# Kernel tuning notes

Measured on AMD Instinct MI355X. Metric: run time of the kernel, lower is better.

The kernel has to match this reference:

```python
import jax, jax.numpy as jnp
import numpy as np

B, SEQ_LEN, IN_DIM = 16, 1024, 768
R = 0.1
PI = 3.1415926


def conv1d(x, w, b):
    # x: [B,C,L], w: [O,I,3], 'same' padding, stride 1
    y = jax.lax.conv_general_dilated(x, w, window_strides=(1,), padding=[(1, 1)],
                                     dimension_numbers=('NCH', 'OIH', 'NCH'))
    return y + b[None, :, None]


def layernorm_cl(x, g, b, eps=1e-5):
    # torch nn.LayerNorm((C, L)): normalize jointly over the last two dims of [B,C,L]
    m = x.mean(axis=(1, 2), keepdims=True)
    v = x.var(axis=(1, 2), keepdims=True)
    return (x - m) / jnp.sqrt(v + eps) * g[None] + b[None]


def setup_inputs() -> dict:
    key = jax.random.key(0)
    ks = jax.random.split(key, 8)
    D, D2, L = IN_DIM, IN_DIM * 2, SEQ_LEN
    sc1 = 1.0 / np.sqrt(D * 3)
    sc2 = 1.0 / np.sqrt(D2 * 3)
    return {
        'feats': jax.random.normal(ks[0], (B, L, D), dtype=jnp.float32),
        'conv1_w': jax.random.normal(ks[1], (D2, D, 3), dtype=jnp.float32) * sc1,
        'conv1_b': jnp.zeros((D2,), jnp.float32),
        'ln1_w': jnp.ones((D2, L), jnp.float32),
        'ln1_b': jnp.zeros((D2, L), jnp.float32),
        'conv2_w': jax.random.normal(ks[2], (D2, D2, 3), dtype=jnp.float32) * sc2,
        'conv2_b': jnp.zeros((D2,), jnp.float32),
        'ln2_w': jnp.ones((D2, L), jnp.float32),
        'ln2_b': jnp.zeros((D2, L), jnp.float32),
        'conv3_w': jax.random.normal(ks[3], (2, D2, 3), dtype=jnp.float32) * sc2,
        'conv3_b': jnp.zeros((2,), jnp.float32),
        'ln3_w': jnp.ones((2, L), jnp.float32),
        'ln3_b': jnp.zeros((2, L), jnp.float32),
    }


def reference(feats, conv1_w, conv1_b, ln1_w, ln1_b, conv2_w, conv2_b, ln2_w, ln2_b,
              conv3_w, conv3_b, ln3_w, ln3_b):
    # NOTE: original uses nn.LeakyReLU(True) -> negative_slope=1.0, i.e. identity.
    x = jnp.transpose(feats, (0, 2, 1))                 # [B,D,L]
    h = layernorm_cl(conv1d(x, conv1_w, conv1_b), ln1_w, ln1_b)
    h = layernorm_cl(conv1d(h, conv2_w, conv2_b), ln2_w, ln2_b)
    h = layernorm_cl(conv1d(h, conv3_w, conv3_b), ln3_w, ln3_b)  # [B,2,L]
    s = jax.nn.softmax(h[:, 0, :], axis=1)              # [B,L]
    w = jax.nn.softmax(h[:, 1, :], axis=1)              # [B,L]
    # Vectorized over all centers i: std[b,i] = R*L*s[b,i]
    std = R * SEQ_LEN * s                               # [B,L]
    pos = jnp.arange(SEQ_LEN, dtype=feats.dtype)
    diff2 = (pos[None, :] - pos[:, None]) ** 2          # [i_center, j]
    c = (2.0 * PI) ** -0.5
    gauss = c / std[:, :, None] * jnp.exp(-diff2[None] / (1e-05 + 2.0 * std[:, :, None] ** 2))
    gauss = gauss / jnp.max(gauss, axis=2, keepdims=True)
    att = gauss * w[:, None, :]                         # [B,L_center,L]
    out = jnp.einsum('bij,bjd->bid', att, feats)        # [B,L,D]
    return out
```

## Files before the change

### kernel.cpp

```cpp
#include <hip/hip_runtime.h>
#include <hip/hip_bf16.h>
#include <cstdint>

#define B_   16
#define L_   1024
#define D_   768
#define D2_  1536

typedef __attribute__((ext_vector_type(8))) short bf16x8;
typedef __attribute__((ext_vector_type(4))) float f32x4;

__device__ __forceinline__ float ldin(const void* p, size_t i, int bf) {
  if (bf) return __bfloat162float(((const __hip_bfloat16*)p)[i]);
  return ((const float*)p)[i];
}
__device__ __forceinline__ unsigned short f2bs(float f) {
  __hip_bfloat16 h = __float2bfloat16(f);
  return *(unsigned short*)&h;
}
__device__ __forceinline__ float bs2f(unsigned short u) {
  __hip_bfloat16 h; *(unsigned short*)&h = u;
  return __bfloat162float(h);
}

__device__ __forceinline__ void gload16(const unsigned short* g, unsigned short* l) {
  __builtin_amdgcn_global_load_lds(
      (const __attribute__((address_space(1))) unsigned int*)g,
      (__attribute__((address_space(3))) unsigned int*)l, 16, 0, 0);
}

__global__ void k_detect(const void* __restrict__ ln1w, int* __restrict__ flag) {
  if (threadIdx.x == 0) {
    unsigned u = *(const unsigned*)ln1w;
    flag[0] = (u == 0x3F800000u) ? 0 : 1;
    flag[1] = 1;
  }
}

__global__ __launch_bounds__(256) void k_check_lnp(const void* __restrict__ g1,
                                                   const void* __restrict__ b1,
                                                   const void* __restrict__ g2,
                                                   const void* __restrict__ b2,
                                                   const void* __restrict__ g3,
                                                   const void* __restrict__ b3,
                                                   const int* __restrict__ flag,
                                                   int* __restrict__ flag2) {
  const int bf = *flag;
  const int n = D2_ * L_;
  bool bad = false;
  for (int i = blockIdx.x * 256 + threadIdx.x; i < n; i += gridDim.x * 256) {
    if (ldin(g1, i, bf) != 1.f || ldin(b1, i, bf) != 0.f ||
        ldin(g2, i, bf) != 1.f || ldin(b2, i, bf) != 0.f) { bad = true; break; }
    if (i < 2 * L_ && (ldin(g3, i, bf) != 1.f || ldin(b3, i, bf) != 0.f)) { bad = true; break; }
  }
  if (bad) atomicAnd(flag2, 0);
}

template<int IC>
__global__ __launch_bounds__(256) void k_wsum(const void* __restrict__ w,
                                              float* __restrict__ wt,
                                              const int* __restrict__ flag) {
  const int bf = *flag;
  const int o = blockIdx.x;
  const size_t base = (size_t)o * IC * 3;
  const int tid = threadIdx.x;
  float s0 = 0.f, s1 = 0.f, s2 = 0.f;
  for (int e = tid; e < 3 * IC; e += 256) {
    float v = ldin(w, base + e, bf);
    int t = e % 3;
    if (t == 0) s0 += v;
    else if (t == 1) s1 += v;
    else s2 += v;
  }
#pragma unroll
  for (int off = 32; off > 0; off >>= 1) {
    s0 += __shfl_down(s0, off);
    s1 += __shfl_down(s1, off);
    s2 += __shfl_down(s2, off);
  }
  __shared__ float red[4][3];
  const int lane = tid & 63, wv = tid >> 6;
  if (lane == 0) { red[wv][0] = s0; red[wv][1] = s1; red[wv][2] = s2; }
  __syncthreads();
  if (tid == 0) {
    wt[o]            = red[0][0] + red[1][0] + red[2][0] + red[3][0];
    wt[D2_ + o]      = red[0][1] + red[1][1] + red[2][1] + red[3][1];
    wt[2 * D2_ + o]  = red[0][2] + red[1][2] + red[2][2] + red[3][2];
  }
}

__global__ void k_wsum3(const void* __restrict__ w3, float* __restrict__ wt3,
                        const int* __restrict__ flag) {
  const int bf = *flag;
  const int tid = threadIdx.x;
  float acc[6] = {0.f, 0.f, 0.f, 0.f, 0.f, 0.f};
  for (int c = tid; c < D2_; c += 256)
#pragma unroll
    for (int ch = 0; ch < 2; ++ch)
#pragma unroll
      for (int t = 0; t < 3; ++t)
        acc[ch * 3 + t] += ldin(w3, ((size_t)ch * D2_ + c) * 3 + t, bf);
  __shared__ float red[6][256];
#pragma unroll
  for (int k = 0; k < 6; ++k) red[k][tid] = acc[k];
  __syncthreads();
  if (tid < 6) {
    float s = 0.f;
    for (int i = 0; i < 256; ++i) s += red[tid][i];
    wt3[tid] = s;
  }
}

__global__ __launch_bounds__(256) void k_cvt_x(const void* __restrict__ in,
                                               unsigned short* __restrict__ out,
                                               const int* __restrict__ flag) {
  const int bf = *flag;
  const size_t total = (size_t)B_ * (L_ + 2) * D_;
  for (size_t i = (size_t)blockIdx.x * 256 + threadIdx.x; i < total; i += (size_t)gridDim.x * 256) {
    size_t b = i / ((L_ + 2) * D_);
    size_t rem = i - b * ((size_t)(L_ + 2) * D_);
    int pr = (int)(rem / D_);
    int ci = (int)(rem - (size_t)pr * D_);
    float v = 0.f;
    if (pr >= 1 && pr <= L_) v = ldin(in, (b * L_ + pr - 1) * D_ + ci, bf);
    out[i] = f2bs(v);
  }
}

template<int IC>
__global__ __launch_bounds__(256) void k_cvt_w(const void* __restrict__ w,
                                               unsigned short* __restrict__ wp,
                                               const int* __restrict__ flag) {
  const int bf = *flag;
  const int n = D2_ * 3 * IC;
  for (int e = blockIdx.x * 256 + threadIdx.x; e < n; e += gridDim.x * 256) {
    int o = e / (3 * IC); int rem = e - o * 3 * IC;
    int t = rem / IC;     int ci = rem - t * IC;
    wp[e] = f2bs(ldin(w, ((size_t)o * IC + ci) * 3 + t, bf));
  }
}

__global__ __launch_bounds__(256) void k_cvt_lnp(const void* __restrict__ src,
                                                 unsigned short* __restrict__ dst,
                                                 const int* __restrict__ flag,
                                                 const int* __restrict__ flag2) {
  if (*flag2) return;
  const int bf = *flag;
  __shared__ float t[32][33];
  const int l0 = blockIdx.x * 32, c0 = blockIdx.y * 32;
  const int tx = threadIdx.x, ty = threadIdx.y;
#pragma unroll
  for (int k = 0; k < 4; ++k)
    t[ty + k * 8][tx] = ldin(src, (size_t)(c0 + ty + k * 8) * L_ + l0 + tx, bf);
  __syncthreads();
#pragma unroll
  for (int k = 0; k < 4; ++k)
    dst[(size_t)(l0 + ty + k * 8) * D2_ + c0 + tx] = f2bs(t[tx][ty + k * 8]);
}

__global__ __launch_bounds__(256) void k_zero_hpad(unsigned short* __restrict__ hbp, int G) {
  int i = blockIdx.x * 256 + threadIdx.x;
  int per = 2 * D2_;
  if (i >= G * per) return;
  int lb = i / per; int rem = i - lb * per;
  int w = rem / D2_; int c = rem - w * D2_;
  hbp[((size_t)lb * (L_ + 2) + (size_t)w * (L_ + 1)) * D2_ + c] = 0;
}

template<int IC, bool FOLD>
__global__ __launch_bounds__(512, 2) void k_conv_mfma(const unsigned short* __restrict__ x,
                                                      const unsigned short* __restrict__ wp,
                                                      const void* __restrict__ bias,
                                                      unsigned short* __restrict__ hout,
                                                      float* __restrict__ part,
                                                      const float* __restrict__ statp,
                                                      const float* __restrict__ wt,
                                                      const int* __restrict__ flag,
                                                      const int* __restrict__ flag2, int b0) {
  __shared__ __attribute__((aligned(16))) unsigned short Xs0[258 * 32];
  __shared__ __attribute__((aligned(16))) unsigned short Xs1[258 * 32];
  __shared__ __attribute__((aligned(16))) unsigned short Ws0[3 * 128 * 32];
  __shared__ __attribute__((aligned(16))) unsigned short Ws1[3 * 128 * 32];
  __shared__ float rs[8], rss[8];
  const int l0 = blockIdx.x * 256, o0 = blockIdx.y * 128, lb = blockIdx.z;
  const int tid = threadIdx.x;
  const int lane = tid & 63, wid = tid >> 6;
  const int wm = wid >> 1, wn = wid & 1;
  const int lr = lane & 15, lg = lane >> 4;

  f32x4 acc[4][4];
#pragma unroll
  for (int m = 0; m < 4; ++m)
#pragma unroll
    for (int n = 0; n < 4; ++n)
      acc[m][n] = (f32x4){0.f, 0.f, 0.f, 0.f};

  const int sx = ((1 + (tid >> 2)) >> 1) & 3;
  const int sw = ((tid >> 2) >> 1) & 3;
  const unsigned short* xbase = x + ((size_t)lb * (L_ + 2) + l0 + 1 + (tid >> 2)) * IC
                                  + (size_t)((tid & 3) ^ sx) * 8;
  const unsigned short* wbase = wp + (size_t)(o0 + (tid >> 2)) * 3 * IC
                                   + (size_t)((tid & 3) ^ sw) * 8;
  const int hr = (tid >> 2) * 257, hcs = tid & 3;
  const unsigned short* hbase = x + ((size_t)lb * (L_ + 2) + l0 + hr) * IC + hcs * 8;

  auto STAGE = [&](unsigned short* Xd, unsigned short* Wd, int ci) {
#pragma unroll
    for (int k = 0; k < 2; ++k)
      gload16(xbase + ci + (size_t)k * 128 * IC, Xd + 32 + tid * 8 + k * 4096);
#pragma unroll
    for (int k = 0; k < 3; ++k)
      gload16(wbase + ci + (size_t)k * IC, Wd + tid * 8 + k * 4096);
  };
  auto COMPUTE = [&](const unsigned short* Xd, const unsigned short* Wd) {
    const int pb = (((lr >> 1) & 3) ^ lg) * 8;
#pragma unroll
    for (int t = 0; t < 3; ++t) {
      const int pa = ((((lr + t) >> 1) & 3) ^ lg) * 8;
      bf16x8 b[4];
#pragma unroll
      for (int n = 0; n < 4; ++n)
        b[n] = *(const bf16x8*)&Wd[(t * 128 + wn * 64 + n * 16 + lr) * 32 + pb];
      __builtin_amdgcn_s_setprio(1);
#pragma unroll
      for (int m = 0; m < 4; ++m) {
        bf16x8 a = *(const bf16x8*)&Xd[(wm * 64 + m * 16 + lr + t) * 32 + pa];
#pragma unroll
        for (int n = 0; n < 4; ++n)
          acc[m][n] = __builtin_amdgcn_mfma_f32_16x16x32_bf16(a, b[n], acc[m][n], 0, 0, 0);
      }
      __builtin_amdgcn_s_setprio(0);
    }
  };

  bf16x8 hreg = {0, 0, 0, 0, 0, 0, 0, 0};
  if (tid < 8) hreg = *(const bf16x8*)(hbase + 0);
  STAGE(Xs0, Ws0, 0);
  if (tid < 8) *(bf16x8*)(Xs0 + hr * 32 + hcs * 8) = hreg;
  asm volatile("s_waitcnt vmcnt(0) lgkmcnt(0)" ::: "memory");
  __builtin_amdgcn_s_barrier();

  for (int ci0 = 0; ci0 < IC; ci0 += 64) {
    {
      const int cin = ci0 + 32;
      if (tid < 8) hreg = *(const bf16x8*)(hbase + cin);
      STAGE(Xs1, Ws1, cin);
      COMPUTE(Xs0, Ws0);
      if (tid < 8) *(bf16x8*)(Xs1 + hr * 32 + hcs * 8) = hreg;
      asm volatile("s_waitcnt vmcnt(0) lgkmcnt(0)" ::: "memory");
      __builtin_amdgcn_s_barrier();
    }
    {
      const int cin = ci0 + 64;
      const bool more = cin < IC;
      if (more) {
        if (tid < 8) hreg = *(const bf16x8*)(hbase + cin);
        STAGE(Xs0, Ws0, cin);
      }
      COMPUTE(Xs1, Ws1);
      if (more) {
        if (tid < 8) *(bf16x8*)(Xs0 + hr * 32 + hcs * 8) = hreg;
        asm volatile("s_waitcnt vmcnt(0) lgkmcnt(0)" ::: "memory");
        __builtin_amdgcn_s_barrier();
      }
    }
  }

  const int bf = *flag;
  const bool fold = FOLD && (*flag2 != 0);
  float r1 = 1.f, m1r = 0.f;
  if (fold) {
    float m1 = statp[(b0 + lb) * 2];
    r1 = statp[(b0 + lb) * 2 + 1];
    m1r = -m1 * r1;
  }
  float s = 0.f, ss = 0.f;
  unsigned short* hb = hout + ((size_t)lb * (L_ + 2) + 1) * D2_;
#pragma unroll
  for (int n = 0; n < 4; ++n) {
    int oo = o0 + wn * 64 + n * 16 + lr;
    float bv = ldin(bias, oo, bf);
    float w0 = 0.f, w2 = 0.f, csum = 0.f;
    if (fold) {
      w0 = m1r * wt[oo];
      w2 = m1r * wt[2 * D2_ + oo];
      csum = w0 + m1r * wt[D2_ + oo] + w2;
    }
#pragma unroll
    for (int m = 0; m < 4; ++m) {
      int lbase = l0 + wm * 64 + m * 16 + lg * 4;
#pragma unroll
      for (int j = 0; j < 4; ++j) {
        int l = lbase + j;
        float v;
        if (fold) {
          float c = csum;
          if (l == 0) c -= w0;
          if (l == L_ - 1) c -= w2;
          v = r1 * acc[m][n][j] + c + bv;
        } else {
          v = acc[m][n][j] + bv;
        }
        hb[(size_t)l * D2_ + oo] = f2bs(v);
        s += v; ss += v * v;
      }
    }
  }
#pragma unroll
  for (int o = 32; o > 0; o >>= 1) { s += __shfl_down(s, o); ss += __shfl_down(ss, o); }
  if (lane == 0) { rs[wid] = s; rss[wid] = ss; }
  __syncthreads();
  if (tid == 0) {
    float S = 0.f, SS = 0.f;
#pragma unroll
    for (int w = 0; w < 8; ++w) { S += rs[w]; SS += rss[w]; }
    size_t pi = ((size_t)(b0 + lb) * 48 + blockIdx.y * 4 + blockIdx.x) * 2;
    part[pi]     = S;
    part[pi + 1] = SS;
  }
}

__global__ void k_stats_final(const float* __restrict__ part, float* __restrict__ stat,
                              int NP, float invN, int b0) {
  const int b = b0 + blockIdx.x;
  float s = 0.f, ss = 0.f;
  for (int p = threadIdx.x; p < NP; p += blockDim.x) {
    s  += part[(size_t)(b * NP + p) * 2];
    ss += part[(size_t)(b * NP + p) * 2 + 1];
  }
#pragma unroll
  for (int o = 32; o > 0; o >>= 1) { s += __shfl_down(s, o); ss += __shfl_down(ss, o); }
  __shared__ float rs[2], rss[2];
  int lane = threadIdx.x & 63, wv = threadIdx.x >> 6;
  if (lane == 0) { rs[wv] = s; rss[wv] = ss; }
  __syncthreads();
  if (threadIdx.x == 0) {
    float m = (rs[0] + rs[1]) * invN;
    float var = (rss[0] + rss[1]) * invN - m * m;
    stat[b * 2] = m;
    stat[b * 2 + 1] = rsqrtf(var + 1e-5f);
  }
}

__global__ __launch_bounds__(256) void k_ln_inplace(unsigned short* __restrict__ hbp,
                                                    const unsigned short* __restrict__ gp,
                                                    const unsigned short* __restrict__ bp,
                                                    const float* __restrict__ stat,
                                                    const int* __restrict__ flag2, int b0) {
  if (*flag2) return;
  const int lb = blockIdx.y;
  const float m = stat[(b0 + lb) * 2], rstd = stat[(b0 + lb) * 2 + 1];
  const int per8 = D2_ * L_ / 8;
  unsigned short* h = hbp + ((size_t)lb * (L_ + 2) + 1) * D2_;
  for (int e = blockIdx.x * 256 + threadIdx.x; e < per8; e += gridDim.x * 256) {
    bf16x8 v = *(bf16x8*)(h + (size_t)e * 8);
    bf16x8 g = *(const bf16x8*)(gp + (size_t)e * 8);
    bf16x8 bb = *(const bf16x8*)(bp + (size_t)e * 8);
    bf16x8 o;
#pragma unroll
    for (int j = 0; j < 8; ++j)
      o[j] = (short)f2bs((bs2f((unsigned short)v[j]) - m) * rstd * bs2f((unsigned short)g[j])
                         + bs2f((unsigned short)bb[j]));
    *(bf16x8*)(h + (size_t)e * 8) = o;
  }
}

__global__ __launch_bounds__(256) void k_conv3b(const unsigned short* __restrict__ hbp,
                                                const void* __restrict__ w3,
                                                const void* __restrict__ b3,
                                                float* __restrict__ y3,
                                                const float* __restrict__ stat,
                                                const float* __restrict__ wt3,
                                                const int* __restrict__ flag,
                                                const int* __restrict__ flag2, int b0) {
  __shared__ unsigned short w3s[2 * 3 * D2_];
  const int bf = *flag;
  const int lb = blockIdx.y, gb = b0 + lb;
  const int tid = threadIdx.x, lane = tid & 63, wid = tid >> 6;
  for (int e = tid; e < 2 * 3 * D2_; e += 256) {
    int ch = e / (3 * D2_); int rem = e - ch * 3 * D2_;
    int t = rem / D2_;      int c = rem - t * D2_;
    w3s[e] = f2bs(ldin(w3, ((size_t)ch * D2_ + c) * 3 + t, bf));
  }
  __syncthreads();
  const int l = blockIdx.x * 4 + wid;
  float a0 = 0.f, a1 = 0.f;
#pragma unroll
  for (int t = 0; t < 3; ++t) {
    const unsigned short* hr = hbp + ((size_t)lb * (L_ + 2) + l + t) * D2_;
    const unsigned short* w0 = w3s + t * D2_;
    const unsigned short* w1 = w3s + (3 + t) * D2_;
#pragma unroll
    for (int i = 0; i < 3; ++i) {
      int c0 = (i * 64 + lane) * 8;
      bf16x8 hv  = *(const bf16x8*)(hr + c0);
      bf16x8 wv0 = *(const bf16x8*)(w0 + c0);
      bf16x8 wv1 = *(const bf16x8*)(w1 + c0);
#pragma unroll
      for (int j = 0; j < 8; ++j) {
        float h = bs2f((unsigned short)hv[j]);
        a0 += h * bs2f((unsigned short)wv0[j]);
        a1 += h * bs2f((unsigned short)wv1[j]);
      }
    }
  }
#pragma unroll
  for (int o = 32; o > 0; o >>= 1) { a0 += __shfl_down(a0, o); a1 += __shfl_down(a1, o); }
  if (lane == 0) {
    float bv0 = ldin(b3, 0, bf), bv1 = ldin(b3, 1, bf);
    float v0, v1;
    if (*flag2) {
      float m2 = stat[gb * 2], r2 = stat[gb * 2 + 1];
      float m2r = -m2 * r2;
      float c0 = m2r * (wt3[0] + wt3[1] + wt3[2]);
      float c1 = m2r * (wt3[3] + wt3[4] + wt3[5]);
      if (l == 0)      { c0 -= m2r * wt3[0]; c1 -= m2r * wt3[3]; }
      if (l == L_ - 1) { c0 -= m2r * wt3[2]; c1 -= m2r * wt3[5]; }
      v0 = r2 * a0 + c0 + bv0;
      v1 = r2 * a1 + c1 + bv1;
    } else {
      v0 = a0 + bv0;
      v1 = a1 + bv1;
    }
    y3[((size_t)gb * 2) * L_ + l]     = v0;
    y3[((size_t)gb * 2 + 1) * L_ + l] = v1;
  }
}

__global__ void k_stats3(const float* __restrict__ y3, float* __restrict__ stat3, int b0) {
  const int b = b0 + blockIdx.x;
  const float* p = y3 + (size_t)b * 2 * L_;
  float s = 0.f, ss = 0.f;
  for (int i = threadIdx.x; i < 2 * L_; i += 256) { float v = p[i]; s += v; ss += v * v; }
#pragma unroll
  for (int o = 32; o > 0; o >>= 1) { s += __shfl_down(s, o); ss += __shfl_down(ss, o); }
  __shared__ float rs[4], rss[4];
  int lane = threadIdx.x & 63, wv = threadIdx.x >> 6;
  if (lane == 0) { rs[wv] = s; rss[wv] = ss; }
  __syncthreads();
  if (threadIdx.x == 0) {
    float invN = 1.f / (2 * L_);
    float m = (rs[0] + rs[1] + rs[2] + rs[3]) * invN;
    float var = (rss[0] + rss[1] + rss[2] + rss[3]) * invN - m * m;
    stat3[b * 2] = m;
    stat3[b * 2 + 1] = rsqrtf(var + 1e-5f);
  }
}

__global__ __launch_bounds__(256) void k_softmax(const float* __restrict__ y3,
                                                 const void* __restrict__ g,
                                                 const void* __restrict__ bt,
                                                 const float* __restrict__ stat3,
                                                 float* __restrict__ sw,
                                                 const int* __restrict__ flag, int b0) {
  const int bf = *flag;
  const int ch = blockIdx.x, gb = b0 + blockIdx.y, tid = threadIdx.x;
  const float m = stat3[gb * 2], rstd = stat3[gb * 2 + 1];
  const float* yp = y3 + ((size_t)gb * 2 + ch) * L_;
  float z[4];
  float mx = -1e30f;
#pragma unroll
  for (int k = 0; k < 4; ++k) {
    int l = tid + k * 256;
    z[k] = (yp[l] - m) * rstd * ldin(g, (size_t)ch * L_ + l, bf) + ldin(bt, (size_t)ch * L_ + l, bf);
    mx = fmaxf(mx, z[k]);
  }
#pragma unroll
  for (int o = 32; o > 0; o >>= 1) mx = fmaxf(mx, __shfl_xor(mx, o));
  __shared__ float red[4];
  int lane = tid & 63, wv = tid >> 6;
  if (lane == 0) red[wv] = mx;
  __syncthreads();
  mx = fmaxf(fmaxf(red[0], red[1]), fmaxf(red[2], red[3]));
  float e[4], sum = 0.f;
#pragma unroll
  for (int k = 0; k < 4; ++k) { e[k] = __expf(z[k] - mx); sum += e[k]; }
#pragma unroll
  for (int o = 32; o > 0; o >>= 1) sum += __shfl_xor(sum, o);
  __shared__ float red2[4];
  if (lane == 0) red2[wv] = sum;
  __syncthreads();
  sum = red2[0] + red2[1] + red2[2] + red2[3];
  float inv = 1.f / sum;
#pragma unroll
  for (int k = 0; k < 4; ++k) {
    int l = tid + k * 256;
    sw[((size_t)ch * B_ + gb) * L_ + l] = e[k] * inv;
  }
}

__global__ __launch_bounds__(256) void k_attn(const float* __restrict__ sw,
                                              const void* __restrict__ feats,
                                              void* __restrict__ out,
                                              const int* __restrict__ flag) {
  const int i = blockIdx.x, b = blockIdx.y, tid = threadIdx.x;
  const float s = sw[(size_t)b * L_ + i];
  const float* wv = sw + (size_t)B_ * L_ + (size_t)b * L_;
  const float stdv = 102.4f * s;
  const float denom = 1e-5f + 2.f * stdv * stdv;
  const float inv = 1.f / denom;
  int r = (int)ceilf(sqrtf(30.f * denom));
  int jlo = i - r; if (jlo < 0) jlo = 0;
  int jhi = i + r; if (jhi > L_ - 1) jhi = L_ - 1;
  float a0 = 0.f, a1 = 0.f, a2 = 0.f;
  const int bf = *flag;
  if (bf) {
    const __hip_bfloat16* fb = (const __hip_bfloat16*)feats + (size_t)b * L_ * D_ + tid;
    for (int j = jlo; j <= jhi; ++j) {
      float d = (float)(j - i);
      float gz = __expf(-d * d * inv) * wv[j];
      const __hip_bfloat16* f = fb + (size_t)j * D_;
      a0 += gz * __bfloat162float(f[0]);
      a1 += gz * __bfloat162float(f[256]);
      a2 += gz * __bfloat162float(f[512]);
    }
    __hip_bfloat16* op = (__hip_bfloat16*)out + ((size_t)b * L_ + i) * D_ + tid;
    op[0]   = __float2bfloat16(a0);
    op[256] = __float2bfloat16(a1);
    op[512] = __float2bfloat16(a2);
  } else {
    const float* fb = (const float*)feats + (size_t)b * L_ * D_ + tid;
    for (int j = jlo; j <= jhi; ++j) {
      float d = (float)(j - i);
      float gz = __expf(-d * d * inv) * wv[j];
      const float* f = fb + (size_t)j * D_;
      a0 += gz * f[0];
      a1 += gz * f[256];
      a2 += gz * f[512];
    }
    float* op = (float*)out + ((size_t)b * L_ + i) * D_ + tid;
    op[0] = a0; op[256] = a1; op[512] = a2;
  }
}

extern "C" void kernel_launch(void* const* d_in, const int* in_sizes, int n_in,
                              void* d_out, int out_size, void* d_ws, size_t ws_size,
                              hipStream_t stream) {
  (void)in_sizes; (void)n_in; (void)out_size;
  char* wsb = (char*)d_ws;
  size_t off = 0;
  auto alloc = [&](size_t bytes) -> char* {
    char* p = wsb + off;
    off += (bytes + 255) & ~(size_t)255;
    return p;
  };
  unsigned short* xbp  = (unsigned short*)alloc((size_t)B_ * (L_ + 2) * D_ * 2);
  unsigned short* wp1  = (unsigned short*)alloc((size_t)D2_ * 3 * D_ * 2);
  unsigned short* wp2  = (unsigned short*)alloc((size_t)D2_ * 3 * D2_ * 2);
  unsigned short* lp1w = (unsigned short*)alloc((size_t)D2_ * L_ * 2);
  unsigned short* lp1b = (unsigned short*)alloc((size_t)D2_ * L_ * 2);
  unsigned short* lp2w = (unsigned short*)alloc((size_t)D2_ * L_ * 2);
  unsigned short* lp2b = (unsigned short*)alloc((size_t)D2_ * L_ * 2);
  float* y3   = (float*)alloc((size_t)B_ * 2 * L_ * 4);
  float* swb  = (float*)alloc((size_t)2 * B_ * L_ * 4);
  float* part = (float*)alloc((size_t)B_ * 48 * 2 * 4);
  float* stat = (float*)alloc((size_t)B_ * 2 * 4);
  float* st3  = (float*)alloc((size_t)B_ * 2 * 4);
  float* wt2  = (float*)alloc((size_t)3 * D2_ * 4);
  float* wt3  = (float*)alloc(6 * 4);
  int*   flag = (int*)alloc(16);
  int*   flag2 = flag + 1;
  const size_t fixed = off;

  int G = 1;
  const int cand[5] = {16, 8, 4, 2, 1};
  for (int k = 0; k < 5; ++k) {
    size_t need = fixed + (size_t)cand[k] * (size_t)(L_ + 2) * D2_ * 2 * 2 + 1024;
    if (need <= ws_size) { G = cand[k]; break; }
  }
  unsigned short* Hbp1 = (unsigned short*)alloc((size_t)G * (L_ + 2) * D2_ * 2);
  unsigned short* Hbp2 = (unsigned short*)alloc((size_t)G * (L_ + 2) * D2_ * 2);

  k_detect<<<1, 64, 0, stream>>>(d_in[3], flag);
  k_check_lnp<<<1024, 256, 0, stream>>>(d_in[3], d_in[4], d_in[7], d_in[8],
                                        d_in[11], d_in[12], flag, flag2);

  k_cvt_x<<<2048, 256, 0, stream>>>(d_in[0], xbp, flag);
  k_cvt_w<768><<<2048, 256, 0, stream>>>(d_in[1], wp1, flag);
  k_cvt_w<1536><<<2048, 256, 0, stream>>>(d_in[5], wp2, flag);
  k_wsum<1536><<<D2_, 256, 0, stream>>>(d_in[5], wt2, flag);
  k_wsum3<<<1, 256, 0, stream>>>(d_in[9], wt3, flag);
  dim3 tg(32, 48), tb(32, 8);
  k_cvt_lnp<<<tg, tb, 0, stream>>>(d_in[3], lp1w, flag, flag2);
  k_cvt_lnp<<<tg, tb, 0, stream>>>(d_in[4], lp1b, flag, flag2);
  k_cvt_lnp<<<tg, tb, 0, stream>>>(d_in[7], lp2w, flag, flag2);
  k_cvt_lnp<<<tg, tb, 0, stream>>>(d_in[8], lp2b, flag, flag2);
  k_zero_hpad<<<(G * 2 * D2_ + 255) / 256, 256, 0, stream>>>(Hbp1, G);
  k_zero_hpad<<<(G * 2 * D2_ + 255) / 256, 256, 0, stream>>>(Hbp2, G);

  const float invN = 1.f / (float)(D2_ * L_);
  for (int b0 = 0; b0 < B_; b0 += G) {
    k_conv_mfma<768, false><<<dim3(4, 12, G), 512, 0, stream>>>(
        xbp + (size_t)b0 * (L_ + 2) * D_, wp1, d_in[2], Hbp1, part,
        stat, wt2, flag, flag2, b0);
    k_stats_final<<<G, 128, 0, stream>>>(part, stat, 48, invN, b0);
    k_ln_inplace<<<dim3(768, G), 256, 0, stream>>>(Hbp1, lp1w, lp1b, stat, flag2, b0);

    k_conv_mfma<1536, true><<<dim3(4, 12, G), 512, 0, stream>>>(
        Hbp1, wp2, d_in[6], Hbp2, part, stat, wt2, flag, flag2, b0);
    k_stats_final<<<G, 128, 0, stream>>>(part, stat, 48, invN, b0);
    k_ln_inplace<<<dim3(768, G), 256, 0, stream>>>(Hbp2, lp2w, lp2b, stat, flag2, b0);

    k_conv3b<<<dim3(L_ / 4, G), 256, 0, stream>>>(Hbp2, d_in[9], d_in[10], y3,
                                                  stat, wt3, flag, flag2, b0);
    k_stats3<<<G, 256, 0, stream>>>(y3, st3, b0);
    k_softmax<<<dim3(2, G), 256, 0, stream>>>(y3, d_in[11], d_in[12], st3, swb, flag, b0);
  }

  k_attn<<<dim3(L_, B_), 256, 0, stream>>>(swb, d_in[0], d_out, flag);
}
```

Baseline: 482.4 us.

## Halve conv block to 4 waves with 128x64 warp tiles and single weight buffer

The MFMA conv kernel now runs 256 threads per block instead of 512, each wave computing an 8x4 grid of 16x16 tiles (128 rows by 64 columns), which doubles register reuse of the B fragments. The weight tile is single-buffered, with an extra barrier before it is refilled, freeing LDS. The input conversion kernel is vectorised to 8 elements per thread, and the four layernorm-parameter transposes are merged into one launch. The larger accumulator footprint raises register pressure, and the added barrier exposes the weight load latency.

```diff
diff --git a/kernel.cpp b/kernel.cpp
--- a/kernel.cpp
+++ b/kernel.cpp
@@ -115,15 +115,27 @@
                                                unsigned short* __restrict__ out,
                                                const int* __restrict__ flag) {
   const int bf = *flag;
-  const size_t total = (size_t)B_ * (L_ + 2) * D_;
-  for (size_t i = (size_t)blockIdx.x * 256 + threadIdx.x; i < total; i += (size_t)gridDim.x * 256) {
-    size_t b = i / ((L_ + 2) * D_);
-    size_t rem = i - b * ((size_t)(L_ + 2) * D_);
-    int pr = (int)(rem / D_);
-    int ci = (int)(rem - (size_t)pr * D_);
-    float v = 0.f;
-    if (pr >= 1 && pr <= L_) v = ldin(in, (b * L_ + pr - 1) * D_ + ci, bf);
-    out[i] = f2bs(v);
+  const int NG = B_ * (L_ + 2) * (D_ / 8);
+  for (int i = blockIdx.x * 256 + threadIdx.x; i < NG; i += gridDim.x * 256) {
+    int b = i / ((L_ + 2) * (D_ / 8));
+    int rem = i - b * ((L_ + 2) * (D_ / 8));
+    int pr = rem / (D_ / 8);
+    int ci0 = (rem - pr * (D_ / 8)) * 8;
+    bf16x8 o = {0, 0, 0, 0, 0, 0, 0, 0};
+    if (pr >= 1 && pr <= L_) {
+      size_t src = ((size_t)b * L_ + pr - 1) * D_ + ci0;
+      if (bf) {
+        o = *(const bf16x8*)((const unsigned short*)in + src);
+      } else {
+        const float4 v0 = *(const float4*)((const float*)in + src);
+        const float4 v1 = *(const float4*)((const float*)in + src + 4);
+        o[0] = (short)f2bs(v0.x); o[1] = (short)f2bs(v0.y);
+        o[2] = (short)f2bs(v0.z); o[3] = (short)f2bs(v0.w);
+        o[4] = (short)f2bs(v1.x); o[5] = (short)f2bs(v1.y);
+        o[6] = (short)f2bs(v1.z); o[7] = (short)f2bs(v1.w);
+      }
+    }
+    *(bf16x8*)(out + (size_t)i * 8) = o;
   }
 }
 
@@ -140,15 +152,28 @@
   }
 }
 
-__global__ __launch_bounds__(256) void k_cvt_lnp(const void* __restrict__ src,
-                                                 unsigned short* __restrict__ dst,
-                                                 const int* __restrict__ flag,
-                                                 const int* __restrict__ flag2) {
+__global__ __launch_bounds__(256) void k_cvt_lnp4(const void* __restrict__ s0,
+                                                  const void* __restrict__ s1,
+                                                  const void* __restrict__ s2,
+                                                  const void* __restrict__ s3,
+                                                  unsigned short* __restrict__ d0,
+                                                  unsigned short* __restrict__ d1,
+                                                  unsigned short* __restrict__ d2,
+                                                  unsigned short* __restrict__ d3,
+                                                  const int* __restrict__ flag,
+                                                  const int* __restrict__ flag2) {
   if (*flag2) return;
+  const void* src; unsigned short* dst;
+  switch (blockIdx.z) {
+    case 0: src = s0; dst = d0; break;
+    case 1: src = s1; dst = d1; break;
+    case 2: src = s2; dst = d2; break;
+    default: src = s3; dst = d3; break;
+  }
   const int bf = *flag;
   __shared__ float t[32][33];
   const int l0 = blockIdx.x * 32, c0 = blockIdx.y * 32;
-  const int tx = threadIdx.x, ty = threadIdx.y;
+  const int tx = threadIdx.x & 31, ty = threadIdx.x >> 5;
 #pragma unroll
   for (int k = 0; k < 4; ++k)
     t[ty + k * 8][tx] = ldin(src, (size_t)(c0 + ty + k * 8) * L_ + l0 + tx, bf);
@@ -168,7 +193,7 @@
 }
 
 template<int IC, bool FOLD>
-__global__ __launch_bounds__(512, 2) void k_conv_mfma(const unsigned short* __restrict__ x,
+__global__ __launch_bounds__(256, 2) void k_conv_mfma(const unsigned short* __restrict__ x,
                                                       const unsigned short* __restrict__ wp,
                                                       const void* __restrict__ bias,
                                                       unsigned short* __restrict__ hout,
@@ -179,24 +204,23 @@
                                                       const int* __restrict__ flag2, int b0) {
   __shared__ __attribute__((aligned(16))) unsigned short Xs0[258 * 32];
   __shared__ __attribute__((aligned(16))) unsigned short Xs1[258 * 32];
-  __shared__ __attribute__((aligned(16))) unsigned short Ws0[3 * 128 * 32];
-  __shared__ __attribute__((aligned(16))) unsigned short Ws1[3 * 128 * 32];
-  __shared__ float rs[8], rss[8];
+  __shared__ __attribute__((aligned(16))) unsigned short Ws[3 * 128 * 32];
+  __shared__ float rs[4], rss[4];
   const int l0 = blockIdx.x * 256, o0 = blockIdx.y * 128, lb = blockIdx.z;
   const int tid = threadIdx.x;
   const int lane = tid & 63, wid = tid >> 6;
   const int wm = wid >> 1, wn = wid & 1;
   const int lr = lane & 15, lg = lane >> 4;
 
-  f32x4 acc[4][4];
-#pragma unroll
-  for (int m = 0; m < 4; ++m)
+  f32x4 acc[8][4];
+#pragma unroll
+  for (int m = 0; m < 8; ++m)
 #pragma unroll
     for (int n = 0; n < 4; ++n)
       acc[m][n] = (f32x4){0.f, 0.f, 0.f, 0.f};
 
   const int sx = ((1 + (tid >> 2)) >> 1) & 3;
-  const int sw = ((tid >> 2) >> 1) & 3;
+  const int sw = (tid >> 3) & 3;
   const unsigned short* xbase = x + ((size_t)lb * (L_ + 2) + l0 + 1 + (tid >> 2)) * IC
                                   + (size_t)((tid & 3) ^ sx) * 8;
   const unsigned short* wbase = wp + (size_t)(o0 + (tid >> 2)) * 3 * IC
@@ -204,38 +228,42 @@
   const int hr = (tid >> 2) * 257, hcs = tid & 3;
   const unsigned short* hbase = x + ((size_t)lb * (L_ + 2) + l0 + hr) * IC + hcs * 8;
 
-  auto STAGE = [&](unsigned short* Xd, unsigned short* Wd, int ci) {
-#pragma unroll
-    for (int k = 0; k < 2; ++k)
-      gload16(xbase + ci + (size_t)k * 128 * IC, Xd + 32 + tid * 8 + k * 4096);
-#pragma unroll
-    for (int k = 0; k < 3; ++k)
-      gload16(wbase + ci + (size_t)k * IC, Wd + tid * 8 + k * 4096);
+  auto STAGE_X = [&](unsigned short* Xd, int ci) {
+#pragma unroll
+    for (int k = 0; k < 4; ++k)
+      gload16(xbase + ci + (size_t)k * 64 * IC, Xd + 32 + tid * 8 + k * 2048);
   };
-  auto COMPUTE = [&](const unsigned short* Xd, const unsigned short* Wd) {
+  auto STAGE_W = [&](int ci) {
+#pragma unroll
+    for (int k = 0; k < 6; ++k)
+      gload16(wbase + ci + (size_t)((k & 1) * 192 + (k >> 1)) * IC, Ws + tid * 8 + k * 2048);
+  };
+  auto COMPUTE = [&](const unsigned short* Xd) {
     const int pb = (((lr >> 1) & 3) ^ lg) * 8;
 #pragma unroll
     for (int t = 0; t < 3; ++t) {
       const int pa = ((((lr + t) >> 1) & 3) ^ lg) * 8;
-      bf16x8 b[4];
+      bf16x8 a[8], b[4];
+#pragma unroll
+      for (int m = 0; m < 8; ++m)
+        a[m] = *(const bf16x8*)&Xd[(wm * 128 + m * 16 + lr + t) * 32 + pa];
 #pragma unroll
       for (int n = 0; n < 4; ++n)
-        b[n] = *(const bf16x8*)&Wd[(t * 128 + wn * 64 + n * 16 + lr) * 32 + pb];
+        b[n] = *(const bf16x8*)&Ws[(t * 128 + wn * 64 + n * 16 + lr) * 32 + pb];
       __builtin_amdgcn_s_setprio(1);
 #pragma unroll
-      for (int m = 0; m < 4; ++m) {
-        bf16x8 a = *(const bf16x8*)&Xd[(wm * 64 + m * 16 + lr + t) * 32 + pa];
+      for (int m = 0; m < 8; ++m)
 #pragma unroll
         for (int n = 0; n < 4; ++n)
-          acc[m][n] = __builtin_amdgcn_mfma_f32_16x16x32_bf16(a, b[n], acc[m][n], 0, 0, 0);
-      }
+          acc[m][n] = __builtin_amdgcn_mfma_f32_16x16x32_bf16(a[m], b[n], acc[m][n], 0, 0, 0);
       __builtin_amdgcn_s_setprio(0);
     }
   };
 
   bf16x8 hreg = {0, 0, 0, 0, 0, 0, 0, 0};
   if (tid < 8) hreg = *(const bf16x8*)(hbase + 0);
-  STAGE(Xs0, Ws0, 0);
+  STAGE_X(Xs0, 0);
+  STAGE_W(0);
   if (tid < 8) *(bf16x8*)(Xs0 + hr * 32 + hcs * 8) = hreg;
   asm volatile("s_waitcnt vmcnt(0) lgkmcnt(0)" ::: "memory");
   __builtin_amdgcn_s_barrier();
@@ -244,8 +272,12 @@
     {
       const int cin = ci0 + 32;
       if (tid < 8) hreg = *(const bf16x8*)(hbase + cin);
-      STAGE(Xs1, Ws1, cin);
-      COMPUTE(Xs0, Ws0);
+      STAGE_X(Xs1, cin);
+      COMPUTE(Xs0);
+      __builtin_amdgcn_sched_barrier(0);
+      __builtin_amdgcn_s_barrier();
+      __builtin_amdgcn_sched_barrier(0);
+      STAGE_W(cin);
       if (tid < 8) *(bf16x8*)(Xs1 + hr * 32 + hcs * 8) = hreg;
       asm volatile("s_waitcnt vmcnt(0) lgkmcnt(0)" ::: "memory");
       __builtin_amdgcn_s_barrier();
@@ -255,10 +287,14 @@
       const bool more = cin < IC;
       if (more) {
         if (tid < 8) hreg = *(const bf16x8*)(hbase + cin);
-        STAGE(Xs0, Ws0, cin);
+        STAGE_X(Xs0, cin);
       }
-      COMPUTE(Xs1, Ws1);
+      COMPUTE(Xs1);
       if (more) {
+        __builtin_amdgcn_sched_barrier(0);
+        __builtin_amdgcn_s_barrier();
+        __builtin_amdgcn_sched_barrier(0);
+        STAGE_W(cin);
         if (tid < 8) *(bf16x8*)(Xs0 + hr * 32 + hcs * 8) = hreg;
         asm volatile("s_waitcnt vmcnt(0) lgkmcnt(0)" ::: "memory");
         __builtin_amdgcn_s_barrier();
@@ -287,8 +323,8 @@
       csum = w0 + m1r * wt[D2_ + oo] + w2;
     }
 #pragma unroll
-    for (int m = 0; m < 4; ++m) {
-      int lbase = l0 + wm * 64 + m * 16 + lg * 4;
+    for (int m = 0; m < 8; ++m) {
+      int lbase = l0 + wm * 128 + m * 16 + lg * 4;
 #pragma unroll
       for (int j = 0; j < 4; ++j) {
         int l = lbase + j;
@@ -311,12 +347,9 @@
   if (lane == 0) { rs[wid] = s; rss[wid] = ss; }
   __syncthreads();
   if (tid == 0) {
-    float S = 0.f, SS = 0.f;
-#pragma unroll
-    for (int w = 0; w < 8; ++w) { S += rs[w]; SS += rss[w]; }
     size_t pi = ((size_t)(b0 + lb) * 48 + blockIdx.y * 4 + blockIdx.x) * 2;
-    part[pi]     = S;
-    part[pi + 1] = SS;
+    part[pi]     = rs[0] + rs[1] + rs[2] + rs[3];
+    part[pi + 1] = rss[0] + rss[1] + rss[2] + rss[3];
   }
 }
 
@@ -580,23 +613,20 @@
   k_cvt_w<1536><<<2048, 256, 0, stream>>>(d_in[5], wp2, flag);
   k_wsum<1536><<<D2_, 256, 0, stream>>>(d_in[5], wt2, flag);
   k_wsum3<<<1, 256, 0, stream>>>(d_in[9], wt3, flag);
-  dim3 tg(32, 48), tb(32, 8);
-  k_cvt_lnp<<<tg, tb, 0, stream>>>(d_in[3], lp1w, flag, flag2);
-  k_cvt_lnp<<<tg, tb, 0, stream>>>(d_in[4], lp1b, flag, flag2);
-  k_cvt_lnp<<<tg, tb, 0, stream>>>(d_in[7], lp2w, flag, flag2);
-  k_cvt_lnp<<<tg, tb, 0, stream>>>(d_in[8], lp2b, flag, flag2);
+  k_cvt_lnp4<<<dim3(32, 48, 4), 256, 0, stream>>>(d_in[3], d_in[4], d_in[7], d_in[8],
+                                                  lp1w, lp1b, lp2w, lp2b, flag, flag2);
   k_zero_hpad<<<(G * 2 * D2_ + 255) / 256, 256, 0, stream>>>(Hbp1, G);
   k_zero_hpad<<<(G * 2 * D2_ + 255) / 256, 256, 0, stream>>>(Hbp2, G);
 
   const float invN = 1.f / (float)(D2_ * L_);
   for (int b0 = 0; b0 < B_; b0 += G) {
-    k_conv_mfma<768, false><<<dim3(4, 12, G), 512, 0, stream>>>(
+    k_conv_mfma<768, false><<<dim3(4, 12, G), 256, 0, stream>>>(
         xbp + (size_t)b0 * (L_ + 2) * D_, wp1, d_in[2], Hbp1, part,
         stat, wt2, flag, flag2, b0);
     k_stats_final<<<G, 128, 0, stream>>>(part, stat, 48, invN, b0);
     k_ln_inplace<<<dim3(768, G), 256, 0, stream>>>(Hbp1, lp1w, lp1b, stat, flag2, b0);
 
-    k_conv_mfma<1536, true><<<dim3(4, 12, G), 512, 0, stream>>>(
+    k_conv_mfma<1536, true><<<dim3(4, 12, G), 256, 0, stream>>>(
         Hbp1, wp2, d_in[6], Hbp2, part, stat, wt2, flag, flag2, b0);
     k_stats_final<<<G, 128, 0, stream>>>(part, stat, 48, invN, b0);
     k_ln_inplace<<<dim3(768, G), 256, 0, stream>>>(Hbp2, lp2w, lp2b, stat, flag2, b0);
```

Result: no change. 491.5 us (+1.9%).
